# Kernel tuning notes

Hardware: AMD Instinct MI355X
Metric: run time of the kernel (lower is better)

Reference implementation:

```python
import jax, jax.numpy as jnp
import numpy as np

C = 256
CI = C // 2  # inter_channels
EPS = 1e-5


def _proj(x, w, b):
    # 1x1 conv == channel matmul: w [O,C], x [n,c,h,w] -> [n,o,h,w]
    return jnp.einsum('oc,nchw->nohw', w, x) + b[None, :, None, None]


def setup_inputs() -> dict:
    key = jax.random.key(0)
    ks = jax.random.split(key, 12)
    shp = (4, C, 64, 64)
    s = 1.0 / np.sqrt(C)
    si = 1.0 / np.sqrt(CI)
    return {
        'x': jax.random.normal(ks[0], shp, jnp.float32),
        'y': jax.random.normal(ks[1], shp, jnp.float32),
        'theta_w': jax.random.normal(ks[2], (CI, C), jnp.float32) * s,
        'theta_b': jax.random.normal(ks[3], (CI,), jnp.float32) * s,
        'phi_w': jax.random.normal(ks[4], (CI, C), jnp.float32) * s,
        'phi_b': jax.random.normal(ks[5], (CI,), jnp.float32) * s,
        'g_w': jax.random.normal(ks[6], (CI, C), jnp.float32) * s,
        'g_b': jax.random.normal(ks[7], (CI,), jnp.float32) * s,
        'rec_w': jax.random.normal(ks[8], (C, CI), jnp.float32) * si,
        'rec_b': jax.random.normal(ks[9], (C,), jnp.float32) * si,
        'gamma': jnp.ones((C,), jnp.float32),
        'beta': jnp.zeros((C,), jnp.float32),
    }


def reference(x, y, theta_w, theta_b, phi_w, phi_b, g_w, g_b, rec_w, rec_b, gamma, beta):
    n, c, h, w = x.shape
    hw = h * w
    # projections (1x1 convs)
    g_x = _proj(x, g_w, g_b).reshape(n, CI, hw).transpose(0, 2, 1)        # [n,HW,CI]
    theta_x = _proj(x, theta_w, theta_b).reshape(n, CI, hw).transpose(0, 2, 1)  # [n,HW,CI]
    phi_y = _proj(y, phi_w, phi_b).reshape(n, CI, hw)                     # [n,CI,HW]
    # attention: QK^T -> softmax -> AV
    attn = jax.nn.softmax(jnp.einsum('nqc,nck->nqk', theta_x, phi_y), axis=-1)  # [n,HW,HW]
    out = jnp.einsum('nqk,nkc->nqc', attn, g_x)                           # [n,HW,CI]
    out = out.transpose(0, 2, 1).reshape(n, CI, h, w)
    out = _proj(out, rec_w, rec_b)                                        # [n,C,h,w]
    # BatchNorm2d (training-mode forward: batch stats over N,H,W; biased var)
    mean = out.mean(axis=(0, 2, 3))
    var = out.var(axis=(0, 2, 3))
    out = gamma[None, :, None, None] * (out - mean[None, :, None, None]) * jax.lax.rsqrt(var + EPS)[None, :, None, None] + beta[None, :, None, None]
    return x + out
```

## Files before the change

### kernel.cpp

```cpp
#include <hip/hip_runtime.h>
#include <math.h>

#define EPSV 1e-5f

typedef __attribute__((ext_vector_type(8))) _Float16 f16x8;
typedef __attribute__((ext_vector_type(4))) float f32x4;

typedef __attribute__((address_space(1))) const unsigned int as1_u32;
typedef __attribute__((address_space(3))) unsigned int as3_u32;

static __device__ __forceinline__ unsigned packh2(float a, float b) {
  auto v = __builtin_amdgcn_cvt_pkrtz(a, b);
  return __builtin_bit_cast(unsigned, v);
}

__global__ __launch_bounds__(256) void pack_w(const float* __restrict__ tw,
                                              const float* __restrict__ pw,
                                              const float* __restrict__ gw,
                                              const float* __restrict__ rw,
                                              _Float16* __restrict__ w16) {
  int i = blockIdx.x * 256 + threadIdx.x;
  const float* s = i < 32768 ? tw : (i < 65536 ? pw : (i < 98304 ? gw : rw));
  w16[i] = (_Float16)s[i & 32767];
}

__global__ __launch_bounds__(256) void pack_xy(const float* __restrict__ x,
                                               const float* __restrict__ y,
                                               _Float16* __restrict__ xt) {
  const int n = blockIdx.y, s = blockIdx.z;
  const int g = blockIdx.x * 256 + threadIdx.x;
  const int p = g & 4095, c8 = g >> 12;
  const float* src = (s ? y : x) + ((size_t)n * 256 + c8 * 8) * 4096 + p;
  f16x8 v;
#pragma unroll
  for (int j = 0; j < 8; ++j) v[j] = (_Float16)src[(size_t)j * 4096];
  *(f16x8*)(xt + ((size_t)(s * 4 + n) * 4096 + p) * 256 + c8 * 8) = v;
}

__global__ __launch_bounds__(256) void proj_kernel(
    const _Float16* __restrict__ xt, const _Float16* __restrict__ w16,
    const float* __restrict__ tb, const float* __restrict__ pb,
    const float* __restrict__ gb, _Float16* __restrict__ th16,
    _Float16* __restrict__ ph16, _Float16* __restrict__ g16) {
  const int ptile = blockIdx.x;
  const int z = blockIdx.y;
  const int pr = z >> 2, n = z & 3;
  const int p0 = ptile * 128;
  const int tid = threadIdx.x, wv = tid >> 6, lane = tid & 63, lg = lane >> 4, lr = lane & 15;

  __shared__ __align__(16) char sB[65536];

  const int srcn = (pr == 1 ? 4 : 0) + n;
  const char* src = (const char*)(xt + ((size_t)srcn * 4096 + p0) * 256);
#pragma unroll
  for (int ps = 0; ps < 16; ++ps) {
    int L = ps * 4096 + tid * 16;
    int row = L >> 9, col = L & 511;
    __builtin_amdgcn_global_load_lds((as1_u32*)(src + (size_t)row * 512 + (col ^ ((row & 7) << 4))),
                                     (as3_u32*)(sB + L), 16, 0, 0);
  }
  const _Float16* wp = w16 + pr * 32768;
  const float* bp = pr == 0 ? tb : (pr == 1 ? pb : gb);

  if (pr != 1) {
    const int o0 = wv * 32;
    f16x8 a[2][8];
#pragma unroll
    for (int mf = 0; mf < 2; ++mf)
#pragma unroll
      for (int kc = 0; kc < 8; ++kc)
        a[mf][kc] = *(const f16x8*)(wp + (size_t)(o0 + mf * 16 + lr) * 256 + kc * 32 + lg * 8);
    __syncthreads();
    f32x4 acc[2][8];
#pragma unroll
    for (int mf = 0; mf < 2; ++mf)
#pragma unroll
      for (int nf = 0; nf < 8; ++nf) acc[mf][nf] = f32x4{0.f, 0.f, 0.f, 0.f};
#pragma unroll
    for (int kc = 0; kc < 8; ++kc) {
      f16x8 bf[8];
#pragma unroll
      for (int nf = 0; nf < 8; ++nf)
        bf[nf] = *(const f16x8*)(sB + (nf * 16 + lr) * 512 + ((kc * 64 + lg * 16) ^ ((lr & 7) << 4)));
#pragma unroll
      for (int mf = 0; mf < 2; ++mf)
#pragma unroll
        for (int nf = 0; nf < 8; ++nf)
          acc[mf][nf] = __builtin_amdgcn_mfma_f32_16x16x32_f16(a[mf][kc], bf[nf], acc[mf][nf], 0, 0, 0);
    }
    _Float16* out = (pr == 0 ? th16 : g16) + (size_t)n * 128 * 4096;
#pragma unroll
    for (int mf = 0; mf < 2; ++mf)
#pragma unroll
      for (int r = 0; r < 4; ++r) {
        int o = o0 + mf * 16 + lg * 4 + r;
        float bias = bp[o];
#pragma unroll
        for (int nf = 0; nf < 8; ++nf)
          out[(size_t)o * 4096 + p0 + nf * 16 + lr] = (_Float16)(acc[mf][nf][r] + bias);
      }
  } else {
    __syncthreads();
    const int pw0 = wv * 32;
    f32x4 acc[2][8];
#pragma unroll
    for (int mf = 0; mf < 2; ++mf)
#pragma unroll
      for (int nf = 0; nf < 8; ++nf) acc[mf][nf] = f32x4{0.f, 0.f, 0.f, 0.f};
#pragma unroll 2
    for (int kc = 0; kc < 8; ++kc) {
      f16x8 bf[8];
#pragma unroll
      for (int nf = 0; nf < 8; ++nf)
        bf[nf] = *(const f16x8*)(wp + (size_t)(nf * 16 + lr) * 256 + kc * 32 + lg * 8);
      f16x8 af[2];
#pragma unroll
      for (int mf = 0; mf < 2; ++mf)
        af[mf] = *(const f16x8*)(sB + (pw0 + mf * 16 + lr) * 512 + ((kc * 64 + lg * 16) ^ ((lr & 7) << 4)));
#pragma unroll
      for (int mf = 0; mf < 2; ++mf)
#pragma unroll
        for (int nf = 0; nf < 8; ++nf)
          acc[mf][nf] = __builtin_amdgcn_mfma_f32_16x16x32_f16(af[mf], bf[nf], acc[mf][nf], 0, 0, 0);
    }
    _Float16* out = ph16 + (size_t)n * 4096 * 128;
#pragma unroll
    for (int mf = 0; mf < 2; ++mf)
#pragma unroll
      for (int r = 0; r < 4; ++r) {
        int p = p0 + pw0 + mf * 16 + lg * 4 + r;
#pragma unroll
        for (int nf = 0; nf < 8; ++nf) {
          int o = nf * 16 + lr;
          out[(size_t)p * 128 + o] = (_Float16)(acc[mf][nf][r] + bp[o]);
        }
      }
  }
}

__global__ __launch_bounds__(512) void attn_kernel(
    const _Float16* __restrict__ th16, const _Float16* __restrict__ ph16,
    const _Float16* __restrict__ g16, _Float16* __restrict__ o16) {
  const int lin = blockIdx.x;
  const int xcd = lin & 7;
  const int n = xcd >> 1;
  const int qt = ((lin >> 3) << 1) | (xcd & 1);
  const int q0 = qt * 64;
  const int tid = threadIdx.x;
  const int wv = tid >> 6, lane = tid & 63, lg = lane >> 4, lr = lane & 15;
  const int half = wv & 1, qsub = wv >> 1;

  __shared__ __align__(16) char smem[147456];
#define KBUF(h, b) (smem + ((h)*2 + (b)) * 16384)
#define GBUF(h, b) (smem + 65536 + ((h)*2 + (b)) * 16384)
  char* pB = smem + 131072 + wv * 2048;

  const _Float16* thn = th16 + (size_t)n * 128 * 4096;
  const char* phn = (const char*)(ph16 + (size_t)n * 4096 * 128);
  const char* ggn = (const char*)(g16 + (size_t)n * 128 * 4096);

  const char* ksrc = phn + (tid >> 4) * 256 + (((tid & 15) * 16) ^ (((tid >> 4) & 7) << 4));
  const char* gsrc = ggn + (size_t)(tid >> 3) * 8192 + (((tid & 7) * 16) ^ (((tid >> 3) & 7) << 4));

#define STAGE(KT, B)                                                                     \
  do {                                                                                   \
    _Pragma("unroll") for (int h_ = 0; h_ < 2; ++h_) {                                   \
      const char* ks = ksrc + (size_t)(h_ * 2048 + (KT) * 64) * 256;                     \
      const char* gs = gsrc + (size_t)(h_ * 2048 + (KT) * 64) * 2;                       \
      char* kd = KBUF(h_, B) + tid * 16;                                                 \
      char* gd = GBUF(h_, B) + tid * 16;                                                 \
      __builtin_amdgcn_global_load_lds((as1_u32*)ks, (as3_u32*)kd, 16, 0, 0);            \
      __builtin_amdgcn_global_load_lds((as1_u32*)(ks + 8192), (as3_u32*)(kd + 8192), 16, 0, 0); \
      __builtin_amdgcn_global_load_lds((as1_u32*)gs, (as3_u32*)gd, 16, 0, 0);            \
      __builtin_amdgcn_global_load_lds((as1_u32*)(gs + 524288), (as3_u32*)(gd + 8192), 16, 0, 0); \
    }                                                                                    \
  } while (0)

  const int q = q0 + qsub * 16 + lr;
  f16x8 qf[4];
#pragma unroll
  for (int ch = 0; ch < 4; ++ch)
#pragma unroll
    for (int j = 0; j < 8; ++j)
      qf[ch][j] = thn[(size_t)(ch * 32 + lg * 8 + j) * 4096 + q];

  const int swzk = (lr & 7) << 4;
  const int swzp = (lr & 15) << 3;

  f32x4 acc[8];
#pragma unroll
  for (int of = 0; of < 8; ++of) acc[of] = f32x4{0.f, 0.f, 0.f, 0.f};
  float mrow = -INFINITY, lrow = 0.f;

  STAGE(0, 0);
  __syncthreads();

  for (int kt = 0; kt < 32; ++kt) {
    const int b = kt & 1;
    if (kt < 31) STAGE(kt + 1, b ^ 1);

    const char* kb = KBUF(half, b);
    f32x4 s[4];
    __builtin_amdgcn_s_setprio(1);
#pragma unroll
    for (int cf = 0; cf < 4; ++cf) {
      const char* krow = kb + (cf * 16 + lr) * 256;
      f32x4 sv = f32x4{0.f, 0.f, 0.f, 0.f};
#pragma unroll
      for (int ch = 0; ch < 4; ++ch) {
        f16x8 kf = *(const f16x8*)(krow + ((ch * 64 + lg * 16) ^ swzk));
        sv = __builtin_amdgcn_mfma_f32_16x16x32_f16(kf, qf[ch], sv, 0, 0, 0);
      }
      s[cf] = sv;
    }
    __builtin_amdgcn_s_setprio(0);

    float mt = s[0][0];
#pragma unroll
    for (int cf = 0; cf < 4; ++cf)
#pragma unroll
      for (int r = 0; r < 4; ++r) mt = fmaxf(mt, s[cf][r]);
    mt = fmaxf(mt, __shfl_xor(mt, 16));
    mt = fmaxf(mt, __shfl_xor(mt, 32));
    if (!__all(mt <= mrow + 8.0f)) {
      float mnew = fmaxf(mrow, mt);
      float sc = __expf(mrow - mnew);
#pragma unroll
      for (int of = 0; of < 8; ++of) acc[of] *= sc;
      lrow *= sc;
      mrow = mnew;
    }
    float psum = 0.f;
    char* prow = pB + lr * 128;
#pragma unroll
    for (int cf = 0; cf < 4; ++cf) {
      float p0 = __expf(s[cf][0] - mrow);
      float p1 = __expf(s[cf][1] - mrow);
      float p2 = __expf(s[cf][2] - mrow);
      float p3 = __expf(s[cf][3] - mrow);
      psum += (p0 + p1) + (p2 + p3);
      unsigned long long w = (unsigned long long)packh2(p0, p1) |
                             ((unsigned long long)packh2(p2, p3) << 32);
      *(unsigned long long*)(prow + ((cf * 32 + lg * 8) ^ swzp)) = w;
    }
    psum += __shfl_xor(psum, 16);
    psum += __shfl_xor(psum, 32);
    lrow += psum;

    const char* gb = GBUF(half, b);
    __builtin_amdgcn_s_setprio(1);
#pragma unroll
    for (int kc = 0; kc < 2; ++kc) {
      int b0 = kc * 64 + lg * 16;
      unsigned long long w0 = *(const unsigned long long*)(prow + (b0 ^ swzp));
      unsigned long long w1 = *(const unsigned long long*)(prow + ((b0 + 8) ^ swzp));
      f16x8 pf;
      unsigned* pu = (unsigned*)&pf;
      pu[0] = (unsigned)w0; pu[1] = (unsigned)(w0 >> 32);
      pu[2] = (unsigned)w1; pu[3] = (unsigned)(w1 >> 32);
#pragma unroll
      for (int of = 0; of < 8; ++of) {
        f16x8 gf = *(const f16x8*)(gb + (of * 16 + lr) * 128 + ((kc * 64 + lg * 16) ^ swzk));
        acc[of] = __builtin_amdgcn_mfma_f32_16x16x32_f16(gf, pf, acc[of], 0, 0, 0);
      }
    }
    __builtin_amdgcn_s_setprio(0);
    __syncthreads();
  }

  float* mg = (float*)(smem + qsub * 9216);
  if (half == 1) {
#pragma unroll
    for (int of = 0; of < 8; ++of)
#pragma unroll
      for (int r = 0; r < 4; ++r) mg[lane * 36 + of * 4 + r] = acc[of][r];
    mg[lane * 36 + 32] = mrow;
    mg[lane * 36 + 33] = lrow;
  }
  __syncthreads();
  if (half == 0) {
    float pm = mg[lane * 36 + 32];
    float pl = mg[lane * 36 + 33];
    float mm = fmaxf(mrow, pm);
    float a0 = __expf(mrow - mm), a1 = __expf(pm - mm);
    float inv = 1.0f / (lrow * a0 + pl * a1);
#pragma unroll
    for (int of = 0; of < 8; ++of)
#pragma unroll
      for (int r = 0; r < 4; ++r)
        acc[of][r] = (acc[of][r] * a0 + mg[lane * 36 + of * 4 + r] * a1) * inv;
  }
  __syncthreads();
  if (half == 0) {
    float* ep = (float*)(smem + qsub * 8448);
#pragma unroll
    for (int of = 0; of < 8; ++of)
#pragma unroll
      for (int r = 0; r < 4; ++r) ep[lr * 132 + of * 16 + lg * 4 + r] = acc[of][r];
    char* on = (char*)(o16 + (size_t)n * 4096 * 128);
#pragma unroll
    for (int it = 0; it < 4; ++it) {
      int e = lane + it * 64;
      int qq = e >> 4, c8 = e & 15;
      f32x4 va = *(const f32x4*)(ep + qq * 132 + c8 * 8);
      f32x4 vb = *(const f32x4*)(ep + qq * 132 + c8 * 8 + 4);
      f16x8 h;
#pragma unroll
      for (int j = 0; j < 4; ++j) { h[j] = (_Float16)va[j]; h[4 + j] = (_Float16)vb[j]; }
      *(f16x8*)(on + (size_t)(q0 + qsub * 16 + qq) * 256 + c8 * 16) = h;
    }
  }
#undef STAGE
#undef KBUF
#undef GBUF
}

__global__ __launch_bounds__(256) void rec_kernel(
    const _Float16* __restrict__ o16, const _Float16* __restrict__ rw16,
    const float* __restrict__ rb, float* __restrict__ out,
    float* __restrict__ partial) {
  const int pblk = blockIdx.x;
  const int n = blockIdx.y;
  const int p0 = pblk * 32;
  const int blin = n * 128 + pblk;
  const int tid = threadIdx.x, wv = tid >> 6, lane = tid & 63, lg = lane >> 4, lr = lane & 15;
  __shared__ __align__(16) char sB[8192];
  const char* o16n = (const char*)(o16 + (size_t)n * 4096 * 128);
  const char* srcb = o16n + (size_t)p0 * 256 + (tid >> 4) * 256 +
                     (((tid & 15) * 16) ^ (((tid >> 4) & 7) << 4));
  __builtin_amdgcn_global_load_lds((as1_u32*)srcb, (as3_u32*)(sB + tid * 16), 16, 0, 0);
  __builtin_amdgcn_global_load_lds((as1_u32*)(srcb + 4096), (as3_u32*)(sB + 4096 + tid * 16), 16, 0, 0);

  const int wc0 = wv * 64;
  f16x8 a[4][4];
#pragma unroll
  for (int mf = 0; mf < 4; ++mf)
#pragma unroll
    for (int kc = 0; kc < 4; ++kc)
      a[mf][kc] = *(const f16x8*)(rw16 + (size_t)(wc0 + mf * 16 + lr) * 128 + kc * 32 + lg * 8);
  __syncthreads();

  f32x4 acc[4][2];
#pragma unroll
  for (int mf = 0; mf < 4; ++mf) {
    acc[mf][0] = f32x4{0.f, 0.f, 0.f, 0.f};
    acc[mf][1] = f32x4{0.f, 0.f, 0.f, 0.f};
  }
  const int xorv = (lr & 7) << 4;
#pragma unroll
  for (int kc = 0; kc < 4; ++kc) {
    int cb = (kc * 64 + lg * 16) ^ xorv;
    f16x8 b0 = *(const f16x8*)(sB + lr * 256 + cb);
    f16x8 b1 = *(const f16x8*)(sB + (16 + lr) * 256 + cb);
#pragma unroll
    for (int mf = 0; mf < 4; ++mf) {
      acc[mf][0] = __builtin_amdgcn_mfma_f32_16x16x32_f16(a[mf][kc], b0, acc[mf][0], 0, 0, 0);
      acc[mf][1] = __builtin_amdgcn_mfma_f32_16x16x32_f16(a[mf][kc], b1, acc[mf][1], 0, 0, 0);
    }
  }
  float* pslot = partial + (size_t)blin * 512;
#pragma unroll
  for (int mf = 0; mf < 4; ++mf)
#pragma unroll
    for (int r = 0; r < 4; ++r) {
      int c = wc0 + mf * 16 + lg * 4 + r;
      float bias = rb[c];
      float v0 = acc[mf][0][r] + bias;
      float v1 = acc[mf][1][r] + bias;
      out[((size_t)n * 256 + c) * 4096 + p0 + lr] = v0;
      out[((size_t)n * 256 + c) * 4096 + p0 + 16 + lr] = v1;
      float s = v0 + v1, qd = v0 * v0 + v1 * v1;
      s += __shfl_xor(s, 1); qd += __shfl_xor(qd, 1);
      s += __shfl_xor(s, 2); qd += __shfl_xor(qd, 2);
      s += __shfl_xor(s, 4); qd += __shfl_xor(qd, 4);
      s += __shfl_xor(s, 8); qd += __shfl_xor(qd, 8);
      if (lr == 0) {
        pslot[c] = s;
        pslot[256 + c] = qd;
      }
    }
}

__global__ __launch_bounds__(256) void stats_reduce(const float* __restrict__ partial,
                                                    float* __restrict__ stats) {
  const int j = blockIdx.x * 256 + threadIdx.x;
  float s = 0.f;
#pragma unroll 8
  for (int b = 0; b < 512; ++b) s += partial[(size_t)b * 512 + j];
  stats[j] = s;
}

__global__ __launch_bounds__(256) void bn_kernel(
    const float* __restrict__ x, const float* __restrict__ gamma,
    const float* __restrict__ beta, const float* __restrict__ stats,
    float* __restrict__ out) {
  const size_t i4 = (size_t)blockIdx.x * 256 + threadIdx.x;
  const int c = (int)((i4 >> 10) & 255);
  const float inv = 1.f / 16384.f;
  const float mean = stats[c] * inv;
  const float var = stats[256 + c] * inv - mean * mean;
  const float gm = gamma[c] * rsqrtf(var + EPSV);
  const float bt = beta[c];
  float4 rv = ((const float4*)out)[i4];
  float4 xv = ((const float4*)x)[i4];
  float4 o;
  o.x = xv.x + (rv.x - mean) * gm + bt;
  o.y = xv.y + (rv.y - mean) * gm + bt;
  o.z = xv.z + (rv.z - mean) * gm + bt;
  o.w = xv.w + (rv.w - mean) * gm + bt;
  ((float4*)out)[i4] = o;
}

extern "C" void kernel_launch(void* const* d_in, const int* in_sizes, int n_in,
                              void* d_out, int out_size, void* d_ws, size_t ws_size,
                              hipStream_t stream) {
  const float* x  = (const float*)d_in[0];
  const float* y  = (const float*)d_in[1];
  const float* tw = (const float*)d_in[2];
  const float* tb = (const float*)d_in[3];
  const float* pw = (const float*)d_in[4];
  const float* pb = (const float*)d_in[5];
  const float* gw = (const float*)d_in[6];
  const float* gb = (const float*)d_in[7];
  const float* rw = (const float*)d_in[8];
  const float* rb = (const float*)d_in[9];
  const float* gamma = (const float*)d_in[10];
  const float* beta  = (const float*)d_in[11];
  float* out = (float*)d_out;
  _Float16* xt   = (_Float16*)d_ws;
  _Float16* w16  = xt + 8388608;
  _Float16* th16 = w16 + 131072;
  _Float16* ph16 = th16 + 2097152;
  _Float16* g16  = ph16 + 2097152;
  _Float16* o16  = g16 + 2097152;
  float* partial = (float*)(o16 + 2097152);
  float* stats   = partial + 262144;
  _Float16* rw16 = w16 + 98304;
  pack_w<<<dim3(512), 256, 0, stream>>>(tw, pw, gw, rw, w16);
  pack_xy<<<dim3(512, 4, 2), 256, 0, stream>>>(x, y, xt);
  proj_kernel<<<dim3(32, 12), 256, 0, stream>>>(xt, w16, tb, pb, gb, th16, ph16, g16);
  attn_kernel<<<dim3(256), 512, 0, stream>>>(th16, ph16, g16, o16);
  rec_kernel<<<dim3(128, 4), 256, 0, stream>>>(o16, rw16, rb, out, partial);
  stats_reduce<<<dim3(2), 256, 0, stream>>>(partial, stats);
  bn_kernel<<<dim3(4096), 256, 0, stream>>>(x, gamma, beta, stats, out);
}
```

Measured before the change: 139.6 us.

## Split keys four ways in attention, stream V from global, store rec output as fp16

The attention kernel now splits the key range across four wave groups, with each wave handling two 16-query groups. Each K fragment is reused for two Q tiles, and the four partial softmax states are merged at the end. V (g) fragments are now read directly from global memory instead of being staged in LDS, and the LDS budget and launch bounds change. Separately, the reconstruction output is written as fp16 to a workspace buffer and read back by the BN kernel, which halves that intermediate traffic at some cost in precision. Loading V uncached from global could add latency, and launch_bounds(512,2) with 160KB of LDS cannot actually give two blocks per CU.

```diff
diff --git a/kernel.cpp b/kernel.cpp
--- a/kernel.cpp
+++ b/kernel.cpp
@@ -4,6 +4,7 @@
 #define EPSV 1e-5f
 
 typedef __attribute__((ext_vector_type(8))) _Float16 f16x8;
+typedef __attribute__((ext_vector_type(4))) _Float16 f16x4;
 typedef __attribute__((ext_vector_type(4))) float f32x4;
 
 typedef __attribute__((address_space(1))) const unsigned int as1_u32;
@@ -138,7 +139,7 @@
   }
 }
 
-__global__ __launch_bounds__(512) void attn_kernel(
+__global__ __launch_bounds__(512, 2) void attn_kernel(
     const _Float16* __restrict__ th16, const _Float16* __restrict__ ph16,
     const _Float16* __restrict__ g16, _Float16* __restrict__ o16) {
   const int lin = blockIdx.x;
@@ -148,176 +149,213 @@
   const int q0 = qt * 64;
   const int tid = threadIdx.x;
   const int wv = tid >> 6, lane = tid & 63, lg = lane >> 4, lr = lane & 15;
-  const int half = wv & 1, qsub = wv >> 1;
-
-  __shared__ __align__(16) char smem[147456];
-#define KBUF(h, b) (smem + ((h)*2 + (b)) * 16384)
-#define GBUF(h, b) (smem + 65536 + ((h)*2 + (b)) * 16384)
-  char* pB = smem + 131072 + wv * 2048;
+  const int quarter = wv & 3, qsub = wv >> 2;
+
+  __shared__ __align__(16) char smem[163840];
 
   const _Float16* thn = th16 + (size_t)n * 128 * 4096;
   const char* phn = (const char*)(ph16 + (size_t)n * 4096 * 128);
   const char* ggn = (const char*)(g16 + (size_t)n * 128 * 4096);
 
-  const char* ksrc = phn + (tid >> 4) * 256 + (((tid & 15) * 16) ^ (((tid >> 4) & 7) << 4));
-  const char* gsrc = ggn + (size_t)(tid >> 3) * 8192 + (((tid & 7) * 16) ^ (((tid >> 3) & 7) << 4));
-
 #define STAGE(KT, B)                                                                     \
   do {                                                                                   \
-    _Pragma("unroll") for (int h_ = 0; h_ < 2; ++h_) {                                   \
-      const char* ks = ksrc + (size_t)(h_ * 2048 + (KT) * 64) * 256;                     \
-      const char* gs = gsrc + (size_t)(h_ * 2048 + (KT) * 64) * 2;                       \
-      char* kd = KBUF(h_, B) + tid * 16;                                                 \
-      char* gd = GBUF(h_, B) + tid * 16;                                                 \
-      __builtin_amdgcn_global_load_lds((as1_u32*)ks, (as3_u32*)kd, 16, 0, 0);            \
-      __builtin_amdgcn_global_load_lds((as1_u32*)(ks + 8192), (as3_u32*)(kd + 8192), 16, 0, 0); \
-      __builtin_amdgcn_global_load_lds((as1_u32*)gs, (as3_u32*)gd, 16, 0, 0);            \
-      __builtin_amdgcn_global_load_lds((as1_u32*)(gs + 524288), (as3_u32*)(gd + 8192), 16, 0, 0); \
+    _Pragma("unroll") for (int i_ = 0; i_ < 8; ++i_) {                                   \
+      const int c_ = wv * 8 + i_;                                                        \
+      const int qq_ = c_ >> 4, sub_ = c_ & 15;                                           \
+      const int pos_ = sub_ * 4 + (lane >> 4);                                           \
+      const char* src_ = phn + (size_t)(qq_ * 1024 + (KT) * 64 + pos_) * 256 +           \
+                         (((lane & 15) * 16) ^ ((pos_ & 7) << 4));                       \
+      char* dst_ = smem + (qq_ * 2 + (B)) * 16384 + sub_ * 1024 + lane * 16;             \
+      __builtin_amdgcn_global_load_lds((as1_u32*)src_, (as3_u32*)dst_, 16, 0, 0);        \
     }                                                                                    \
   } while (0)
 
-  const int q = q0 + qsub * 16 + lr;
-  f16x8 qf[4];
-#pragma unroll
-  for (int ch = 0; ch < 4; ++ch)
-#pragma unroll
-    for (int j = 0; j < 8; ++j)
-      qf[ch][j] = thn[(size_t)(ch * 32 + lg * 8 + j) * 4096 + q];
+  f16x8 qf[2][4];
+#pragma unroll
+  for (int qg = 0; qg < 2; ++qg)
+#pragma unroll
+    for (int ch = 0; ch < 4; ++ch)
+#pragma unroll
+      for (int j = 0; j < 8; ++j)
+        qf[qg][ch][j] = thn[(size_t)(ch * 32 + lg * 8 + j) * 4096 + q0 + qsub * 32 + qg * 16 + lr];
 
   const int swzk = (lr & 7) << 4;
   const int swzp = (lr & 15) << 3;
-
-  f32x4 acc[8];
-#pragma unroll
-  for (int of = 0; of < 8; ++of) acc[of] = f32x4{0.f, 0.f, 0.f, 0.f};
-  float mrow = -INFINITY, lrow = 0.f;
+  char* pW = smem + 131072 + wv * 4096;
+
+  f32x4 acc[2][8];
+#pragma unroll
+  for (int qg = 0; qg < 2; ++qg)
+#pragma unroll
+    for (int of = 0; of < 8; ++of) acc[qg][of] = f32x4{0.f, 0.f, 0.f, 0.f};
+  float mrow[2] = {-INFINITY, -INFINITY}, lrow[2] = {0.f, 0.f};
 
   STAGE(0, 0);
   __syncthreads();
 
-  for (int kt = 0; kt < 32; ++kt) {
+  for (int kt = 0; kt < 16; ++kt) {
     const int b = kt & 1;
-    if (kt < 31) STAGE(kt + 1, b ^ 1);
-
-    const char* kb = KBUF(half, b);
-    f32x4 s[4];
+    if (kt < 15) STAGE(kt + 1, b ^ 1);
+
+    const char* kb = smem + (quarter * 2 + b) * 16384;
+    f32x4 s[4][2];
+#pragma unroll
+    for (int cf = 0; cf < 4; ++cf) {
+      s[cf][0] = f32x4{0.f, 0.f, 0.f, 0.f};
+      s[cf][1] = f32x4{0.f, 0.f, 0.f, 0.f};
+    }
     __builtin_amdgcn_s_setprio(1);
 #pragma unroll
     for (int cf = 0; cf < 4; ++cf) {
       const char* krow = kb + (cf * 16 + lr) * 256;
-      f32x4 sv = f32x4{0.f, 0.f, 0.f, 0.f};
 #pragma unroll
       for (int ch = 0; ch < 4; ++ch) {
         f16x8 kf = *(const f16x8*)(krow + ((ch * 64 + lg * 16) ^ swzk));
-        sv = __builtin_amdgcn_mfma_f32_16x16x32_f16(kf, qf[ch], sv, 0, 0, 0);
-      }
-      s[cf] = sv;
+        s[cf][0] = __builtin_amdgcn_mfma_f32_16x16x32_f16(kf, qf[0][ch], s[cf][0], 0, 0, 0);
+        s[cf][1] = __builtin_amdgcn_mfma_f32_16x16x32_f16(kf, qf[1][ch], s[cf][1], 0, 0, 0);
+      }
     }
     __builtin_amdgcn_s_setprio(0);
 
-    float mt = s[0][0];
-#pragma unroll
-    for (int cf = 0; cf < 4; ++cf)
-#pragma unroll
-      for (int r = 0; r < 4; ++r) mt = fmaxf(mt, s[cf][r]);
-    mt = fmaxf(mt, __shfl_xor(mt, 16));
-    mt = fmaxf(mt, __shfl_xor(mt, 32));
-    if (!__all(mt <= mrow + 8.0f)) {
-      float mnew = fmaxf(mrow, mt);
-      float sc = __expf(mrow - mnew);
-#pragma unroll
-      for (int of = 0; of < 8; ++of) acc[of] *= sc;
-      lrow *= sc;
-      mrow = mnew;
-    }
-    float psum = 0.f;
-    char* prow = pB + lr * 128;
-#pragma unroll
-    for (int cf = 0; cf < 4; ++cf) {
-      float p0 = __expf(s[cf][0] - mrow);
-      float p1 = __expf(s[cf][1] - mrow);
-      float p2 = __expf(s[cf][2] - mrow);
-      float p3 = __expf(s[cf][3] - mrow);
-      psum += (p0 + p1) + (p2 + p3);
-      unsigned long long w = (unsigned long long)packh2(p0, p1) |
-                             ((unsigned long long)packh2(p2, p3) << 32);
-      *(unsigned long long*)(prow + ((cf * 32 + lg * 8) ^ swzp)) = w;
-    }
-    psum += __shfl_xor(psum, 16);
-    psum += __shfl_xor(psum, 32);
-    lrow += psum;
-
-    const char* gb = GBUF(half, b);
+#pragma unroll
+    for (int qg = 0; qg < 2; ++qg) {
+      float mt = s[0][qg][0];
+#pragma unroll
+      for (int cf = 0; cf < 4; ++cf)
+#pragma unroll
+        for (int r = 0; r < 4; ++r) mt = fmaxf(mt, s[cf][qg][r]);
+      mt = fmaxf(mt, __shfl_xor(mt, 16));
+      mt = fmaxf(mt, __shfl_xor(mt, 32));
+      if (!__all(mt <= mrow[qg] + 8.0f)) {
+        float mnew = fmaxf(mrow[qg], mt);
+        float sc = __expf(mrow[qg] - mnew);
+#pragma unroll
+        for (int of = 0; of < 8; ++of) acc[qg][of] *= sc;
+        lrow[qg] *= sc;
+        mrow[qg] = mnew;
+      }
+      float psum = 0.f;
+      char* prow = pW + qg * 2048 + lr * 128;
+#pragma unroll
+      for (int cf = 0; cf < 4; ++cf) {
+        float p0 = __expf(s[cf][qg][0] - mrow[qg]);
+        float p1 = __expf(s[cf][qg][1] - mrow[qg]);
+        float p2 = __expf(s[cf][qg][2] - mrow[qg]);
+        float p3 = __expf(s[cf][qg][3] - mrow[qg]);
+        psum += (p0 + p1) + (p2 + p3);
+        unsigned long long w = (unsigned long long)packh2(p0, p1) |
+                               ((unsigned long long)packh2(p2, p3) << 32);
+        *(unsigned long long*)(prow + ((cf * 32 + lg * 8) ^ swzp)) = w;
+      }
+      psum += __shfl_xor(psum, 16);
+      psum += __shfl_xor(psum, 32);
+      lrow[qg] += psum;
+    }
+
+    const size_t gk = (size_t)(quarter * 1024 + kt * 64);
     __builtin_amdgcn_s_setprio(1);
 #pragma unroll
     for (int kc = 0; kc < 2; ++kc) {
-      int b0 = kc * 64 + lg * 16;
-      unsigned long long w0 = *(const unsigned long long*)(prow + (b0 ^ swzp));
-      unsigned long long w1 = *(const unsigned long long*)(prow + ((b0 + 8) ^ swzp));
-      f16x8 pf;
-      unsigned* pu = (unsigned*)&pf;
-      pu[0] = (unsigned)w0; pu[1] = (unsigned)(w0 >> 32);
-      pu[2] = (unsigned)w1; pu[3] = (unsigned)(w1 >> 32);
+      const int b0 = kc * 64 + lg * 16;
+      char* pr0 = pW + lr * 128;
+      char* pr1 = pW + 2048 + lr * 128;
+      unsigned long long a0 = *(unsigned long long*)(pr0 + (b0 ^ swzp));
+      unsigned long long a1 = *(unsigned long long*)(pr0 + ((b0 + 8) ^ swzp));
+      unsigned long long b0q = *(unsigned long long*)(pr1 + (b0 ^ swzp));
+      unsigned long long b1q = *(unsigned long long*)(pr1 + ((b0 + 8) ^ swzp));
+      f16x8 pf0, pf1;
+      {
+        unsigned* u = (unsigned*)&pf0;
+        u[0] = (unsigned)a0; u[1] = (unsigned)(a0 >> 32);
+        u[2] = (unsigned)a1; u[3] = (unsigned)(a1 >> 32);
+      }
+      {
+        unsigned* u = (unsigned*)&pf1;
+        u[0] = (unsigned)b0q; u[1] = (unsigned)(b0q >> 32);
+        u[2] = (unsigned)b1q; u[3] = (unsigned)(b1q >> 32);
+      }
 #pragma unroll
       for (int of = 0; of < 8; ++of) {
-        f16x8 gf = *(const f16x8*)(gb + (of * 16 + lr) * 128 + ((kc * 64 + lg * 16) ^ swzk));
-        acc[of] = __builtin_amdgcn_mfma_f32_16x16x32_f16(gf, pf, acc[of], 0, 0, 0);
+        f16x8 gf = *(const f16x8*)(ggn + ((size_t)(of * 16 + lr) * 4096 + gk + kc * 32 + lg * 8) * 2);
+        acc[0][of] = __builtin_amdgcn_mfma_f32_16x16x32_f16(gf, pf0, acc[0][of], 0, 0, 0);
+        acc[1][of] = __builtin_amdgcn_mfma_f32_16x16x32_f16(gf, pf1, acc[1][of], 0, 0, 0);
       }
     }
     __builtin_amdgcn_s_setprio(0);
     __syncthreads();
   }
 
-  float* mg = (float*)(smem + qsub * 9216);
-  if (half == 1) {
-#pragma unroll
-    for (int of = 0; of < 8; ++of)
-#pragma unroll
-      for (int r = 0; r < 4; ++r) mg[lane * 36 + of * 4 + r] = acc[of][r];
-    mg[lane * 36 + 32] = mrow;
-    mg[lane * 36 + 33] = lrow;
+  float* fsm = (float*)smem;
+  if (quarter != 0) {
+    const int pi = (quarter - 1) * 2 + qsub;
+    float* aslot = fsm + pi * 4096 + lane * 64;
+#pragma unroll
+    for (int qg = 0; qg < 2; ++qg)
+#pragma unroll
+      for (int of = 0; of < 8; ++of) *(f32x4*)(aslot + (qg * 8 + of) * 4) = acc[qg][of];
+    float* ml = fsm + 24576 + (pi * 64 + lane) * 4;
+    ml[0] = mrow[0]; ml[1] = lrow[0]; ml[2] = mrow[1]; ml[3] = lrow[1];
   }
   __syncthreads();
-  if (half == 0) {
-    float pm = mg[lane * 36 + 32];
-    float pl = mg[lane * 36 + 33];
-    float mm = fmaxf(mrow, pm);
-    float a0 = __expf(mrow - mm), a1 = __expf(pm - mm);
-    float inv = 1.0f / (lrow * a0 + pl * a1);
-#pragma unroll
-    for (int of = 0; of < 8; ++of)
-#pragma unroll
-      for (int r = 0; r < 4; ++r)
-        acc[of][r] = (acc[of][r] * a0 + mg[lane * 36 + of * 4 + r] * a1) * inv;
-  }
-  __syncthreads();
-  if (half == 0) {
-    float* ep = (float*)(smem + qsub * 8448);
-#pragma unroll
-    for (int of = 0; of < 8; ++of)
-#pragma unroll
-      for (int r = 0; r < 4; ++r) ep[lr * 132 + of * 16 + lg * 4 + r] = acc[of][r];
+  if (quarter == 0) {
+#pragma unroll
+    for (int qg = 0; qg < 2; ++qg) {
+      float mm = mrow[qg];
+      float pm[3], pl[3];
+#pragma unroll
+      for (int p_ = 0; p_ < 3; ++p_) {
+        const float* ml = fsm + 24576 + ((p_ * 2 + qsub) * 64 + lane) * 4;
+        pm[p_] = ml[qg * 2];
+        pl[p_] = ml[qg * 2 + 1];
+        mm = fmaxf(mm, pm[p_]);
+      }
+      float a0 = __expf(mrow[qg] - mm);
+      float l = lrow[qg] * a0;
+      float aa[3];
+#pragma unroll
+      for (int p_ = 0; p_ < 3; ++p_) {
+        aa[p_] = __expf(pm[p_] - mm);
+        l += pl[p_] * aa[p_];
+      }
+      float inv = 1.0f / l;
+#pragma unroll
+      for (int of = 0; of < 8; ++of) {
+        f32x4 v = acc[qg][of] * a0;
+#pragma unroll
+        for (int p_ = 0; p_ < 3; ++p_) {
+          const f32x4 pv = *(const f32x4*)(fsm + (p_ * 2 + qsub) * 4096 + lane * 64 + (qg * 8 + of) * 4);
+          v += pv * aa[p_];
+        }
+        acc[qg][of] = v * inv;
+      }
+    }
+    float* ep = fsm + 28672 + qsub * 2112;
     char* on = (char*)(o16 + (size_t)n * 4096 * 128);
 #pragma unroll
-    for (int it = 0; it < 4; ++it) {
-      int e = lane + it * 64;
-      int qq = e >> 4, c8 = e & 15;
-      f32x4 va = *(const f32x4*)(ep + qq * 132 + c8 * 8);
-      f32x4 vb = *(const f32x4*)(ep + qq * 132 + c8 * 8 + 4);
-      f16x8 h;
-#pragma unroll
-      for (int j = 0; j < 4; ++j) { h[j] = (_Float16)va[j]; h[4 + j] = (_Float16)vb[j]; }
-      *(f16x8*)(on + (size_t)(q0 + qsub * 16 + qq) * 256 + c8 * 16) = h;
+    for (int qg = 0; qg < 2; ++qg) {
+#pragma unroll
+      for (int of = 0; of < 8; ++of)
+#pragma unroll
+        for (int r = 0; r < 4; ++r) ep[lr * 132 + of * 16 + lg * 4 + r] = acc[qg][of][r];
+#pragma unroll
+      for (int it = 0; it < 4; ++it) {
+        int e = lane + it * 64;
+        int qq = e >> 4, c8 = e & 15;
+        f32x4 va = *(const f32x4*)(ep + qq * 132 + c8 * 8);
+        f32x4 vb = *(const f32x4*)(ep + qq * 132 + c8 * 8 + 4);
+        f16x8 h;
+#pragma unroll
+        for (int j = 0; j < 4; ++j) { h[j] = (_Float16)va[j]; h[4 + j] = (_Float16)vb[j]; }
+        *(f16x8*)(on + (size_t)(q0 + qsub * 32 + qg * 16 + qq) * 256 + c8 * 16) = h;
+      }
     }
   }
 #undef STAGE
-#undef KBUF
-#undef GBUF
 }
 
 __global__ __launch_bounds__(256) void rec_kernel(
     const _Float16* __restrict__ o16, const _Float16* __restrict__ rw16,
-    const float* __restrict__ rb, float* __restrict__ out,
+    const float* __restrict__ rb, _Float16* __restrict__ rec16,
     float* __restrict__ partial) {
   const int pblk = blockIdx.x;
   const int n = blockIdx.y;
@@ -367,8 +405,8 @@
       float bias = rb[c];
       float v0 = acc[mf][0][r] + bias;
       float v1 = acc[mf][1][r] + bias;
-      out[((size_t)n * 256 + c) * 4096 + p0 + lr] = v0;
-      out[((size_t)n * 256 + c) * 4096 + p0 + 16 + lr] = v1;
+      rec16[((size_t)n * 256 + c) * 4096 + p0 + lr] = (_Float16)v0;
+      rec16[((size_t)n * 256 + c) * 4096 + p0 + 16 + lr] = (_Float16)v1;
       float s = v0 + v1, qd = v0 * v0 + v1 * v1;
       s += __shfl_xor(s, 1); qd += __shfl_xor(qd, 1);
       s += __shfl_xor(s, 2); qd += __shfl_xor(qd, 2);
@@ -393,7 +431,7 @@
 __global__ __launch_bounds__(256) void bn_kernel(
     const float* __restrict__ x, const float* __restrict__ gamma,
     const float* __restrict__ beta, const float* __restrict__ stats,
-    float* __restrict__ out) {
+    const _Float16* __restrict__ rec16, float* __restrict__ out) {
   const size_t i4 = (size_t)blockIdx.x * 256 + threadIdx.x;
   const int c = (int)((i4 >> 10) & 255);
   const float inv = 1.f / 16384.f;
@@ -401,13 +439,13 @@
   const float var = stats[256 + c] * inv - mean * mean;
   const float gm = gamma[c] * rsqrtf(var + EPSV);
   const float bt = beta[c];
-  float4 rv = ((const float4*)out)[i4];
+  f16x4 r4 = ((const f16x4*)rec16)[i4];
   float4 xv = ((const float4*)x)[i4];
   float4 o;
-  o.x = xv.x + (rv.x - mean) * gm + bt;
-  o.y = xv.y + (rv.y - mean) * gm + bt;
-  o.z = xv.z + (rv.z - mean) * gm + bt;
-  o.w = xv.w + (rv.w - mean) * gm + bt;
+  o.x = xv.x + ((float)r4[0] - mean) * gm + bt;
+  o.y = xv.y + ((float)r4[1] - mean) * gm + bt;
+  o.z = xv.z + ((float)r4[2] - mean) * gm + bt;
+  o.w = xv.w + ((float)r4[3] - mean) * gm + bt;
   ((float4*)out)[i4] = o;
 }
 
@@ -427,20 +465,21 @@
   const float* gamma = (const float*)d_in[10];
   const float* beta  = (const float*)d_in[11];
   float* out = (float*)d_out;
-  _Float16* xt   = (_Float16*)d_ws;
-  _Float16* w16  = xt + 8388608;
-  _Float16* th16 = w16 + 131072;
-  _Float16* ph16 = th16 + 2097152;
-  _Float16* g16  = ph16 + 2097152;
-  _Float16* o16  = g16 + 2097152;
-  float* partial = (float*)(o16 + 2097152);
-  float* stats   = partial + 262144;
+  _Float16* xt    = (_Float16*)d_ws;
+  _Float16* w16   = xt + 8388608;
+  _Float16* th16  = w16 + 131072;
+  _Float16* ph16  = th16 + 2097152;
+  _Float16* g16   = ph16 + 2097152;
+  _Float16* o16   = g16 + 2097152;
+  _Float16* rec16 = o16 + 2097152;
+  float* partial  = (float*)(rec16 + 4194304);
+  float* stats    = partial + 262144;
   _Float16* rw16 = w16 + 98304;
   pack_w<<<dim3(512), 256, 0, stream>>>(tw, pw, gw, rw, w16);
   pack_xy<<<dim3(512, 4, 2), 256, 0, stream>>>(x, y, xt);
   proj_kernel<<<dim3(32, 12), 256, 0, stream>>>(xt, w16, tb, pb, gb, th16, ph16, g16);
   attn_kernel<<<dim3(256), 512, 0, stream>>>(th16, ph16, g16, o16);
-  rec_kernel<<<dim3(128, 4), 256, 0, stream>>>(o16, rw16, rb, out, partial);
+  rec_kernel<<<dim3(128, 4), 256, 0, stream>>>(o16, rw16, rb, rec16, partial);
   stats_reduce<<<dim3(2), 256, 0, stream>>>(partial, stats);
-  bn_kernel<<<dim3(4096), 256, 0, stream>>>(x, gamma, beta, stats, out);
-}
+  bn_kernel<<<dim3(4096), 256, 0, stream>>>(x, gamma, beta, stats, rec16, out);
+}
```

Result: slower. 170.2 us (+21.9%).
